# Kernel optimization log

Hardware: AMD Instinct MI355X
Metric: run time of the kernel (lower is better)

Reference implementation:

```python
import jax, jax.numpy as jnp
import numpy as np

EPS = 1e-8
LAM = 1.0


def setup_inputs() -> dict:
    key = jax.random.key(0)
    k1, k2 = jax.random.split(key)
    B, H, W = 32, 512, 512
    output = jax.random.normal(k1, (B, 1, H, W), dtype=jnp.float32)
    target = jax.random.normal(k2, (B, 1, H, W), dtype=jnp.float32)
    return {"output": output, "target": target}


def _frc_loss(output, target):
    # squeeze channel dim: (B,1,H,W) -> (B,H,W)
    output = output[:, 0]
    target = target[:, 0]
    B, H, W = output.shape
    rnyquist = H // 2

    # radial index map (H,W): round(sqrt(fx^2 + fy^2)) in pixel-frequency units
    fx = jnp.fft.fftfreq(H, 1.0 / H)
    fy = jnp.fft.fftfreq(W, 1.0 / W)
    X, Y = jnp.meshgrid(fx, fy, indexing='ij')
    radial = jnp.round(jnp.sqrt(X ** 2 + Y ** 2)).astype(jnp.int32)
    # bins > rnyquist were ignored by the original loop -> dump into extra bin
    idx = jnp.where(radial > rnyquist, rnyquist + 1, radial).reshape(-1)  # (H*W,)

    F1 = jnp.fft.fft2(output, norm='forward')  # (B,H,W) complex
    F2 = jnp.fft.fft2(target, norm='forward')

    # per-pixel correlation terms, laid out (HW, B) for segment_sum over leading axis
    a = (F1.real * F2.real + F1.imag * F2.imag).reshape(B, -1).T
    b = (F1.imag * F2.real - F1.real * F2.imag).reshape(B, -1).T
    c1 = (F1.real ** 2 + F1.imag ** 2).reshape(B, -1).T
    c2 = (F2.real ** 2 + F2.imag ** 2).reshape(B, -1).T
    stacked = jnp.stack([a, b, c1, c2], axis=-1)  # (HW, B, 4)

    # single-pass radial-bin segment sum (replaces O(R*H*W) masked loop)
    sums = jax.ops.segment_sum(stacked, idx, num_segments=rnyquist + 2)
    sums = sums[:rnyquist + 1]  # drop overflow bin -> (rnyquist+1, B, 4)
    C_r, C_i, C1, C2 = sums[..., 0], sums[..., 1], sums[..., 2], sums[..., 3]

    frc = jnp.sqrt(C_r ** 2 + C_i ** 2) / (jnp.sqrt(C1 * C2) + EPS)
    return LAM * jnp.mean((1.0 - frc) ** 2)


def reference(output, target):
    return _frc_loss(output, target)
```

## Files before the change

### kernel.cpp

```cpp
#include <hip/hip_runtime.h>
#include <math.h>

#define NIMG 32
#define NB3  771
#define PI_F 3.14159265358979323846f

__device__ __forceinline__ float2 cadd(float2 a, float2 b){ return make_float2(a.x+b.x, a.y+b.y); }
__device__ __forceinline__ float2 csub(float2 a, float2 b){ return make_float2(a.x-b.x, a.y-b.y); }
__device__ __forceinline__ float2 cmul(float2 a, float2 b){ return make_float2(a.x*b.x - a.y*b.y, a.x*b.y + a.y*b.x); }
__device__ __forceinline__ float2 cmul_mi(float2 a){ return make_float2(a.y, -a.x); }
__device__ __forceinline__ float2 tw(const float2* T, int m){ return T[m + (m >> 3)]; }
__device__ __forceinline__ int   sw(int pos){ return pos + (pos >> 3); }

__device__ __forceinline__ void dft8(float2* x) {
    const float c = 0.70710678118654752f;
    float2 u0 = cadd(x[0], x[4]), u1 = cadd(x[1], x[5]);
    float2 u2 = cadd(x[2], x[6]), u3 = cadd(x[3], x[7]);
    float2 v0 = csub(x[0], x[4]);
    float2 d1 = csub(x[1], x[5]);
    float2 v1 = make_float2(c*(d1.x + d1.y), c*(d1.y - d1.x));
    float2 d2 = csub(x[2], x[6]);
    float2 v2 = make_float2(d2.y, -d2.x);
    float2 d3 = csub(x[3], x[7]);
    float2 v3 = make_float2(-c*(d3.x - d3.y), -c*(d3.x + d3.y));
    float2 e0 = cadd(u0,u2), e1 = cadd(u1,u3);
    float2 f0 = csub(u0,u2), f1 = cmul_mi(csub(u1,u3));
    float2 g0 = cadd(v0,v2), g1 = cadd(v1,v3);
    float2 h0 = csub(v0,v2), h1 = cmul_mi(csub(v1,v3));
    x[0] = cadd(e0,e1); x[4] = csub(e0,e1);
    x[2] = cadd(f0,f1); x[6] = csub(f0,f1);
    x[1] = cadd(g0,g1); x[5] = csub(g0,g1);
    x[3] = cadd(h0,h1); x[7] = csub(h0,h1);
}

__device__ __forceinline__ void wave_fft512(float2* X, float2* Sw,
                                            const float2* T, int J) {
    dft8(X);
#pragma unroll
    for (int k = 1; k < 8; ++k) X[k] = cmul(X[k], tw(T, J * k));
    const int jj = J + (J >> 3);
#pragma unroll
    for (int k = 0; k < 8; ++k) Sw[jj + 72*k] = X[k];

    const int j2 = J & 7;
    const int bb = 72 * (J >> 3) + j2;
#pragma unroll
    for (int q = 0; q < 8; ++q) X[q] = Sw[bb + 9*q];
    dft8(X);
#pragma unroll
    for (int k = 1; k < 8; ++k) X[k] = cmul(X[k], tw(T, 8 * j2 * k));
#pragma unroll
    for (int k = 0; k < 8; ++k) Sw[bb + 9*k] = X[k];

#pragma unroll
    for (int q = 0; q < 8; ++q) X[q] = Sw[9*J + q];
    dft8(X);
}

__global__ __launch_bounds__(256, 6) void fft_rows_T(const float* __restrict__ xr,
                                                     const float* __restrict__ yr,
                                                     float2* __restrict__ Zt) {
    __shared__ float2 S[4 * 576];
    __shared__ float2 T[576];
    const int t = threadIdx.x, w = t >> 6, J = t & 63;
    const int im = blockIdx.x >> 6, grp = blockIdx.x & 63;

#pragma unroll
    for (int i = 0; i < 2; ++i) {
        const int m = t + 256 * i;
        float s, c;
        __sincosf(-2.0f * PI_F * (float)m / 512.0f, &s, &c);
        T[m + (m >> 3)] = make_float2(c, s);
    }

    const size_t b0 = ((size_t)(im * 512 + grp * 8 + w)) << 9;
    const size_t b1 = b0 + (4u << 9);
    float2 X0[8], X1[8];
#pragma unroll
    for (int q = 0; q < 8; ++q) {
        X0[q] = make_float2(xr[b0 + J + 64*q], yr[b0 + J + 64*q]);
        X1[q] = make_float2(xr[b1 + J + 64*q], yr[b1 + J + 64*q]);
    }
    __syncthreads();

    float2* Sw = S + w * 576;
    wave_fft512(X0, Sw, T, J);
    wave_fft512(X1, Sw, T, J);

    const int r = ((J & 7) << 3) | (J >> 3);

#pragma unroll
    for (int k = 0; k < 8; ++k) Sw[64*k + r] = X0[k];
    __syncthreads();
    float2 eA[4], eB[4];
#pragma unroll
    for (int j = 0; j < 4; ++j) { eA[j] = S[j*576 + t]; eB[j] = S[j*576 + t + 256]; }
    __syncthreads();

#pragma unroll
    for (int k = 0; k < 8; ++k) Sw[64*k + r] = X1[k];
    __syncthreads();

    const size_t zb = ((size_t)im << 18) + (grp << 3);
    {
        float4* o = (float4*)(Zt + zb + ((size_t)t << 9));
        float2 f0 = S[0*576 + t], f1 = S[1*576 + t];
        float2 f2 = S[2*576 + t], f3 = S[3*576 + t];
        o[0] = make_float4(eA[0].x, eA[0].y, eA[1].x, eA[1].y);
        o[1] = make_float4(eA[2].x, eA[2].y, eA[3].x, eA[3].y);
        o[2] = make_float4(f0.x, f0.y, f1.x, f1.y);
        o[3] = make_float4(f2.x, f2.y, f3.x, f3.y);
    }
    {
        float4* o = (float4*)(Zt + zb + ((size_t)(t + 256) << 9));
        float2 f0 = S[0*576 + t + 256], f1 = S[1*576 + t + 256];
        float2 f2 = S[2*576 + t + 256], f3 = S[3*576 + t + 256];
        o[0] = make_float4(eB[0].x, eB[0].y, eB[1].x, eB[1].y);
        o[1] = make_float4(eB[2].x, eB[2].y, eB[3].x, eB[3].y);
        o[2] = make_float4(f0.x, f0.y, f1.x, f1.y);
        o[3] = make_float4(f2.x, f2.y, f3.x, f3.y);
    }
}

__global__ __launch_bounds__(256) void fft_cols_rings(const float2* __restrict__ Zt,
                                                      float* __restrict__ sums,
                                                      int big) {
    __shared__ float2 S[8 * 576];
    __shared__ float2 T[576];
    __shared__ float  bins[258 * 3];
    const int t = threadIdx.x, w = t >> 6, J = t & 63;
    const int im = blockIdx.x >> 6, g = blockIdx.x & 63;
    const int p = 4 * g + w;

#pragma unroll
    for (int i = 0; i < 2; ++i) {
        const int m = t + 256 * i;
        float s, c;
        __sincosf(-2.0f * PI_F * (float)m / 512.0f, &s, &c);
        T[m + (m >> 3)] = make_float2(c, s);
    }
    for (int i = t; i < 258 * 3; i += 256) bins[i] = 0.0f;

    const int c0 = (p == 0) ? 0   : p;
    const int c1 = (p == 0) ? 256 : 512 - p;
    const float2* rp0 = Zt + ((size_t)im << 18) + ((size_t)c0 << 9);
    const float2* rp1 = Zt + ((size_t)im << 18) + ((size_t)c1 << 9);
    float2 X0[8], X1[8];
#pragma unroll
    for (int q = 0; q < 8; ++q) { X0[q] = rp0[J + 64*q]; X1[q] = rp1[J + 64*q]; }
    __syncthreads();

    float2* A = S + (2*w) * 576;
    float2* B = A + 576;
    const int r  = ((J & 7) << 3) | (J >> 3);
    const int pk = r + (r >> 3);

    wave_fft512(X0, A, T, J);
#pragma unroll
    for (int k = 0; k < 8; ++k) A[72*k + pk] = X0[k];
    wave_fft512(X1, B, T, J);
#pragma unroll
    for (int k = 0; k < 8; ++k) B[72*k + pk] = X1[k];

    const float scale = 1.0f / (512.0f * 512.0f);
    auto pix = [&](float2 zk, float2 zm, float& av, float& c1v, float& c2v) {
        float f1r = 0.5f * (zk.x + zm.x) * scale;
        float f1i = 0.5f * (zk.y - zm.y) * scale;
        float f2r = 0.5f * (zk.y + zm.y) * scale;
        float f2i = 0.5f * (zm.x - zk.x) * scale;
        av  = f1r * f2r + f1i * f2i;
        c1v = f1r * f1r + f1i * f1i;
        c2v = f2r * f2r + f2i * f2i;
    };
    auto flush = [&](int ring, float a, float b, float c) {
        if (ring >= 0 && ring <= 256) {
            unsafeAtomicAdd(&bins[ring*3+0], a);
            unsafeAtomicAdd(&bins[ring*3+1], b);
            unsafeAtomicAdd(&bins[ring*3+2], c);
        }
    };

    if (p == 0) {
        int cur0 = -1, cur1 = -1;
        float a0 = 0, b0 = 0, c0v = 0, a1 = 0, b1 = 0, c1v = 0;
#pragma unroll
        for (int i = 0; i < 8; ++i) {
            const int ky  = 8*J + i;
            const int kyp = (512 - ky) & 511;
            float2 zk0 = A[sw(ky)], zm0 = A[sw(kyp)];
            float2 zk1 = B[sw(ky)], zm1 = B[sw(kyp)];
            const float fk = (ky < 256) ? (float)ky : (float)(ky - 512);
            float av, cv, dv;
            pix(zk0, zm0, av, cv, dv);
            int rr = (int)rintf(fabsf(fk)); if (rr > 256) rr = 257;
            if (rr != cur0) { flush(cur0, a0, b0, c0v); cur0 = rr; a0 = av; b0 = cv; c0v = dv; }
            else            { a0 += av; b0 += cv; c0v += dv; }
            pix(zk1, zm1, av, cv, dv);
            rr = (int)rintf(sqrtf(fk*fk + 65536.0f)); if (rr > 256) rr = 257;
            if (rr != cur1) { flush(cur1, a1, b1, c1v); cur1 = rr; a1 = av; b1 = cv; c1v = dv; }
            else            { a1 += av; b1 += cv; c1v += dv; }
        }
        flush(cur0, a0, b0, c0v);
        flush(cur1, a1, b1, c1v);
    } else {
        const float fy2 = (float)p * (float)p;
        int curR = -1;
        float sA = 0, sB = 0, sC = 0;
#pragma unroll
        for (int i = 0; i < 8; ++i) {
            const int ky  = 8*J + i;
            const int kyp = (512 - ky) & 511;
            float2 zk = A[sw(ky)];
            float2 zm = B[sw(kyp)];
            float a1v, b1v, d1v, a2v, b2v, d2v;
            pix(zk, zm, a1v, b1v, d1v);
            pix(zm, zk, a2v, b2v, d2v);
            const float fk = (ky < 256) ? (float)ky : (float)(ky - 512);
            int rr = (int)rintf(sqrtf(fk*fk + fy2)); if (rr > 256) rr = 257;
            const float aa = a1v + a2v, bb = b1v + b2v, cc = d1v + d2v;
            if (rr != curR) { flush(curR, sA, sB, sC); curR = rr; sA = aa; sB = bb; sC = cc; }
            else            { sA += aa; sB += bb; sC += cc; }
        }
        flush(curR, sA, sB, sC);
    }
    __syncthreads();

    if (big) {
        float* dst = sums + (size_t)blockIdx.x * NB3;
        for (int i = t; i < NB3; i += 256) dst[i] = bins[i];
    } else {
        float* dst = sums + (size_t)(im * 8 + (g & 7)) * NB3;
        for (int i = t; i < NB3; i += 256) unsafeAtomicAdd(&dst[i], bins[i]);
    }
}

__global__ __launch_bounds__(256) void finalize(const float* __restrict__ sums,
                                                float* __restrict__ out, int spi) {
    const int b = blockIdx.x, t = threadIdx.x;
    float acc = 0.0f;
    for (int r = t; r < 257; r += 256) {
        float cr = 0.f, c1 = 0.f, c2 = 0.f;
        for (int s = 0; s < spi; ++s) {
            const float* pp = sums + (size_t)(b * spi + s) * NB3 + r * 3;
            cr += pp[0]; c1 += pp[1]; c2 += pp[2];
        }
        float frc = fabsf(cr) / (sqrtf(c1 * c2) + 1e-8f);
        float d = 1.0f - frc;
        acc += d * d;
    }
#pragma unroll
    for (int off = 32; off > 0; off >>= 1) acc += __shfl_down(acc, off);
    __shared__ float red[4];
    if ((t & 63) == 0) red[t >> 6] = acc;
    __syncthreads();
    if (t == 0)
        unsafeAtomicAdd(out, (red[0] + red[1] + red[2] + red[3]) *
                             (1.0f / (257.0f * (float)NIMG)));
}

extern "C" void kernel_launch(void* const* d_in, const int* in_sizes, int n_in,
                              void* d_out, int out_size, void* d_ws, size_t ws_size,
                              hipStream_t stream) {
    const float* xr = (const float*)d_in[0];
    const float* yr = (const float*)d_in[1];

    float2* Zt = (float2*)d_ws;
    const size_t ztBytes = ((size_t)NIMG << 18) * sizeof(float2);
    float* sums = (float*)((char*)d_ws + ztBytes);
    const int big = (ws_size >= ztBytes + (size_t)2048 * NB3 * sizeof(float)) ? 1 : 0;

    if (!big)
        hipMemsetAsync(sums, 0, (size_t)NIMG * 8 * NB3 * sizeof(float), stream);
    hipMemsetAsync(d_out, 0, sizeof(float), stream);

    fft_rows_T    <<<dim3(NIMG * 64), dim3(256), 0, stream>>>(xr, yr, Zt);
    fft_cols_rings<<<dim3(NIMG * 64), dim3(256), 0, stream>>>(Zt, sums, big);
    finalize      <<<dim3(NIMG), dim3(256), 0, stream>>>(sums, (float*)d_out, big ? 64 : 8);
}
```

Before: 213.9 us.

## Fuse row FFT, column FFT/ring binning and finalize into one persistent kernel

Replaces the three kernel launches and the memsets of sums and output with a single persistent kernel of 512 blocks. The blocks loop over the work units of each stage and meet at software grid barriers built from atomic counters in global memory. This removes launch gaps and the separate memset work, and always uses the atomic 8-slot sums path. The barriers only work if all 512 blocks are resident at once, which is not guaranteed, so the kernel can deadlock. Each stage also now runs at lower parallelism than the earlier 2048-block launches.

Measured after the change: 290.3 us. 1.36x slower.

```diff
diff --git a/kernel.cpp b/kernel.cpp
--- a/kernel.cpp
+++ b/kernel.cpp
@@ -4,13 +4,14 @@
 #define NIMG 32
 #define NB3  771
 #define PI_F 3.14159265358979323846f
+#define GRID 512
 
 __device__ __forceinline__ float2 cadd(float2 a, float2 b){ return make_float2(a.x+b.x, a.y+b.y); }
 __device__ __forceinline__ float2 csub(float2 a, float2 b){ return make_float2(a.x-b.x, a.y-b.y); }
 __device__ __forceinline__ float2 cmul(float2 a, float2 b){ return make_float2(a.x*b.x - a.y*b.y, a.x*b.y + a.y*b.x); }
 __device__ __forceinline__ float2 cmul_mi(float2 a){ return make_float2(a.y, -a.x); }
 __device__ __forceinline__ float2 tw(const float2* T, int m){ return T[m + (m >> 3)]; }
-__device__ __forceinline__ int   sw(int pos){ return pos + (pos >> 3); }
+__device__ __forceinline__ int   swz(int pos){ return pos + (pos >> 3); }
 
 __device__ __forceinline__ void dft8(float2* x) {
     const float c = 0.70710678118654752f;
@@ -57,13 +58,30 @@
     dft8(X);
 }
 
-__global__ __launch_bounds__(256, 6) void fft_rows_T(const float* __restrict__ xr,
-                                                     const float* __restrict__ yr,
-                                                     float2* __restrict__ Zt) {
-    __shared__ float2 S[4 * 576];
+__device__ __forceinline__ void gbar(unsigned* bar, int idx) {
+    __syncthreads();
+    if (threadIdx.x == 0) {
+        __threadfence();
+        atomicAdd(&bar[idx], 1u);
+        while (__hip_atomic_load(&bar[idx], __ATOMIC_RELAXED,
+                                 __HIP_MEMORY_SCOPE_AGENT) < GRID) {
+            __builtin_amdgcn_s_sleep(2);
+        }
+        __threadfence();
+    }
+    __syncthreads();
+}
+
+__global__ __launch_bounds__(256, 2)
+void frc_mega(const float* __restrict__ xr, const float* __restrict__ yr,
+              float2* __restrict__ Zt, float* __restrict__ sums,
+              unsigned* __restrict__ bar, float* __restrict__ out) {
+    __shared__ float2 S[8 * 576];
     __shared__ float2 T[576];
+    __shared__ float  bins[258 * 3];
+    __shared__ float  red[4];
     const int t = threadIdx.x, w = t >> 6, J = t & 63;
-    const int im = blockIdx.x >> 6, grp = blockIdx.x & 63;
+    const int r = ((J & 7) << 3) | (J >> 3);
 
 #pragma unroll
     for (int i = 0; i < 2; ++i) {
@@ -72,190 +90,175 @@
         __sincosf(-2.0f * PI_F * (float)m / 512.0f, &s, &c);
         T[m + (m >> 3)] = make_float2(c, s);
     }
-
-    const size_t b0 = ((size_t)(im * 512 + grp * 8 + w)) << 9;
-    const size_t b1 = b0 + (4u << 9);
-    float2 X0[8], X1[8];
-#pragma unroll
-    for (int q = 0; q < 8; ++q) {
-        X0[q] = make_float2(xr[b0 + J + 64*q], yr[b0 + J + 64*q]);
-        X1[q] = make_float2(xr[b1 + J + 64*q], yr[b1 + J + 64*q]);
-    }
+    for (int i = blockIdx.x * 256 + t; i < NIMG * 8 * NB3; i += GRID * 256)
+        sums[i] = 0.0f;
+    if (blockIdx.x == 0 && t == 0) atomicExch(out, 0.0f);
     __syncthreads();
 
-    float2* Sw = S + w * 576;
-    wave_fft512(X0, Sw, T, J);
-    wave_fft512(X1, Sw, T, J);
-
-    const int r = ((J & 7) << 3) | (J >> 3);
-
-#pragma unroll
-    for (int k = 0; k < 8; ++k) Sw[64*k + r] = X0[k];
-    __syncthreads();
-    float2 eA[4], eB[4];
-#pragma unroll
-    for (int j = 0; j < 4; ++j) { eA[j] = S[j*576 + t]; eB[j] = S[j*576 + t + 256]; }
-    __syncthreads();
-
-#pragma unroll
-    for (int k = 0; k < 8; ++k) Sw[64*k + r] = X1[k];
-    __syncthreads();
-
-    const size_t zb = ((size_t)im << 18) + (grp << 3);
-    {
-        float4* o = (float4*)(Zt + zb + ((size_t)t << 9));
-        float2 f0 = S[0*576 + t], f1 = S[1*576 + t];
-        float2 f2 = S[2*576 + t], f3 = S[3*576 + t];
-        o[0] = make_float4(eA[0].x, eA[0].y, eA[1].x, eA[1].y);
-        o[1] = make_float4(eA[2].x, eA[2].y, eA[3].x, eA[3].y);
-        o[2] = make_float4(f0.x, f0.y, f1.x, f1.y);
-        o[3] = make_float4(f2.x, f2.y, f3.x, f3.y);
-    }
-    {
-        float4* o = (float4*)(Zt + zb + ((size_t)(t + 256) << 9));
-        float2 f0 = S[0*576 + t + 256], f1 = S[1*576 + t + 256];
-        float2 f2 = S[2*576 + t + 256], f3 = S[3*576 + t + 256];
-        o[0] = make_float4(eB[0].x, eB[0].y, eB[1].x, eB[1].y);
-        o[1] = make_float4(eB[2].x, eB[2].y, eB[3].x, eB[3].y);
-        o[2] = make_float4(f0.x, f0.y, f1.x, f1.y);
-        o[3] = make_float4(f2.x, f2.y, f3.x, f3.y);
-    }
-}
-
-__global__ __launch_bounds__(256) void fft_cols_rings(const float2* __restrict__ Zt,
-                                                      float* __restrict__ sums,
-                                                      int big) {
-    __shared__ float2 S[8 * 576];
-    __shared__ float2 T[576];
-    __shared__ float  bins[258 * 3];
-    const int t = threadIdx.x, w = t >> 6, J = t & 63;
-    const int im = blockIdx.x >> 6, g = blockIdx.x & 63;
-    const int p = 4 * g + w;
-
-#pragma unroll
-    for (int i = 0; i < 2; ++i) {
-        const int m = t + 256 * i;
-        float s, c;
-        __sincosf(-2.0f * PI_F * (float)m / 512.0f, &s, &c);
-        T[m + (m >> 3)] = make_float2(c, s);
-    }
-    for (int i = t; i < 258 * 3; i += 256) bins[i] = 0.0f;
-
-    const int c0 = (p == 0) ? 0   : p;
-    const int c1 = (p == 0) ? 256 : 512 - p;
-    const float2* rp0 = Zt + ((size_t)im << 18) + ((size_t)c0 << 9);
-    const float2* rp1 = Zt + ((size_t)im << 18) + ((size_t)c1 << 9);
-    float2 X0[8], X1[8];
-#pragma unroll
-    for (int q = 0; q < 8; ++q) { X0[q] = rp0[J + 64*q]; X1[q] = rp1[J + 64*q]; }
-    __syncthreads();
-
-    float2* A = S + (2*w) * 576;
-    float2* B = A + 576;
-    const int r  = ((J & 7) << 3) | (J >> 3);
-    const int pk = r + (r >> 3);
-
-    wave_fft512(X0, A, T, J);
-#pragma unroll
-    for (int k = 0; k < 8; ++k) A[72*k + pk] = X0[k];
-    wave_fft512(X1, B, T, J);
-#pragma unroll
-    for (int k = 0; k < 8; ++k) B[72*k + pk] = X1[k];
+    for (int u = blockIdx.x; u < 2048; u += GRID) {
+        const int im = u >> 6, grp = u & 63;
+        const size_t b0 = ((size_t)(im * 512 + grp * 8 + w)) << 9;
+        const size_t b1 = b0 + 2048;
+        float2 X0[8], X1[8];
+#pragma unroll
+        for (int q = 0; q < 8; ++q) {
+            X0[q] = make_float2(xr[b0 + J + 64*q], yr[b0 + J + 64*q]);
+            X1[q] = make_float2(xr[b1 + J + 64*q], yr[b1 + J + 64*q]);
+        }
+        float2* Sw = S + w * 576;
+        wave_fft512(X0, Sw, T, J);
+        wave_fft512(X1, Sw, T, J);
+
+#pragma unroll
+        for (int k = 0; k < 8; ++k) Sw[64*k + r] = X0[k];
+        __syncthreads();
+        float2 eA[4], eB[4];
+#pragma unroll
+        for (int j = 0; j < 4; ++j) { eA[j] = S[j*576 + t]; eB[j] = S[j*576 + t + 256]; }
+        __syncthreads();
+#pragma unroll
+        for (int k = 0; k < 8; ++k) Sw[64*k + r] = X1[k];
+        __syncthreads();
+
+        const size_t zb = ((size_t)im << 18) + (grp << 3);
+        {
+            float4* o = (float4*)(Zt + zb + ((size_t)t << 9));
+            float2 f0 = S[0*576 + t], f1 = S[1*576 + t];
+            float2 f2 = S[2*576 + t], f3 = S[3*576 + t];
+            o[0] = make_float4(eA[0].x, eA[0].y, eA[1].x, eA[1].y);
+            o[1] = make_float4(eA[2].x, eA[2].y, eA[3].x, eA[3].y);
+            o[2] = make_float4(f0.x, f0.y, f1.x, f1.y);
+            o[3] = make_float4(f2.x, f2.y, f3.x, f3.y);
+        }
+        {
+            float4* o = (float4*)(Zt + zb + ((size_t)(t + 256) << 9));
+            float2 f0 = S[0*576 + t + 256], f1 = S[1*576 + t + 256];
+            float2 f2 = S[2*576 + t + 256], f3 = S[3*576 + t + 256];
+            o[0] = make_float4(eB[0].x, eB[0].y, eB[1].x, eB[1].y);
+            o[1] = make_float4(eB[2].x, eB[2].y, eB[3].x, eB[3].y);
+            o[2] = make_float4(f0.x, f0.y, f1.x, f1.y);
+            o[3] = make_float4(f2.x, f2.y, f3.x, f3.y);
+        }
+        __syncthreads();
+    }
+
+    gbar(bar, 0);
 
     const float scale = 1.0f / (512.0f * 512.0f);
-    auto pix = [&](float2 zk, float2 zm, float& av, float& c1v, float& c2v) {
-        float f1r = 0.5f * (zk.x + zm.x) * scale;
-        float f1i = 0.5f * (zk.y - zm.y) * scale;
-        float f2r = 0.5f * (zk.y + zm.y) * scale;
-        float f2i = 0.5f * (zm.x - zk.x) * scale;
-        av  = f1r * f2r + f1i * f2i;
-        c1v = f1r * f1r + f1i * f1i;
-        c2v = f2r * f2r + f2i * f2i;
-    };
-    auto flush = [&](int ring, float a, float b, float c) {
-        if (ring >= 0 && ring <= 256) {
-            unsafeAtomicAdd(&bins[ring*3+0], a);
-            unsafeAtomicAdd(&bins[ring*3+1], b);
-            unsafeAtomicAdd(&bins[ring*3+2], c);
-        }
-    };
-
-    if (p == 0) {
-        int cur0 = -1, cur1 = -1;
-        float a0 = 0, b0 = 0, c0v = 0, a1 = 0, b1 = 0, c1v = 0;
-#pragma unroll
-        for (int i = 0; i < 8; ++i) {
-            const int ky  = 8*J + i;
-            const int kyp = (512 - ky) & 511;
-            float2 zk0 = A[sw(ky)], zm0 = A[sw(kyp)];
-            float2 zk1 = B[sw(ky)], zm1 = B[sw(kyp)];
-            const float fk = (ky < 256) ? (float)ky : (float)(ky - 512);
-            float av, cv, dv;
-            pix(zk0, zm0, av, cv, dv);
-            int rr = (int)rintf(fabsf(fk)); if (rr > 256) rr = 257;
-            if (rr != cur0) { flush(cur0, a0, b0, c0v); cur0 = rr; a0 = av; b0 = cv; c0v = dv; }
-            else            { a0 += av; b0 += cv; c0v += dv; }
-            pix(zk1, zm1, av, cv, dv);
-            rr = (int)rintf(sqrtf(fk*fk + 65536.0f)); if (rr > 256) rr = 257;
-            if (rr != cur1) { flush(cur1, a1, b1, c1v); cur1 = rr; a1 = av; b1 = cv; c1v = dv; }
-            else            { a1 += av; b1 += cv; c1v += dv; }
-        }
-        flush(cur0, a0, b0, c0v);
-        flush(cur1, a1, b1, c1v);
-    } else {
-        const float fy2 = (float)p * (float)p;
-        int curR = -1;
-        float sA = 0, sB = 0, sC = 0;
-#pragma unroll
-        for (int i = 0; i < 8; ++i) {
-            const int ky  = 8*J + i;
-            const int kyp = (512 - ky) & 511;
-            float2 zk = A[sw(ky)];
-            float2 zm = B[sw(kyp)];
-            float a1v, b1v, d1v, a2v, b2v, d2v;
-            pix(zk, zm, a1v, b1v, d1v);
-            pix(zm, zk, a2v, b2v, d2v);
-            const float fk = (ky < 256) ? (float)ky : (float)(ky - 512);
-            int rr = (int)rintf(sqrtf(fk*fk + fy2)); if (rr > 256) rr = 257;
-            const float aa = a1v + a2v, bb = b1v + b2v, cc = d1v + d2v;
-            if (rr != curR) { flush(curR, sA, sB, sC); curR = rr; sA = aa; sB = bb; sC = cc; }
-            else            { sA += aa; sB += bb; sC += cc; }
-        }
-        flush(curR, sA, sB, sC);
-    }
-    __syncthreads();
-
-    if (big) {
-        float* dst = sums + (size_t)blockIdx.x * NB3;
-        for (int i = t; i < NB3; i += 256) dst[i] = bins[i];
-    } else {
+    for (int u = blockIdx.x; u < 2048; u += GRID) {
+        const int im = u >> 6, g = u & 63;
+        const int p = 4 * g + w;
+        for (int i = t; i < 258 * 3; i += 256) bins[i] = 0.0f;
+
+        const int c0 = (p == 0) ? 0   : p;
+        const int c1 = (p == 0) ? 256 : 512 - p;
+        const float2* rp0 = Zt + ((size_t)im << 18) + ((size_t)c0 << 9);
+        const float2* rp1 = Zt + ((size_t)im << 18) + ((size_t)c1 << 9);
+        float2 X0[8], X1[8];
+#pragma unroll
+        for (int q = 0; q < 8; ++q) { X0[q] = rp0[J + 64*q]; X1[q] = rp1[J + 64*q]; }
+        __syncthreads();
+
+        float2* A = S + (2*w) * 576;
+        float2* B = A + 576;
+        const int pk = r + (r >> 3);
+        wave_fft512(X0, A, T, J);
+#pragma unroll
+        for (int k = 0; k < 8; ++k) A[72*k + pk] = X0[k];
+        wave_fft512(X1, B, T, J);
+#pragma unroll
+        for (int k = 0; k < 8; ++k) B[72*k + pk] = X1[k];
+
+        auto pix = [&](float2 zk, float2 zm, float& av, float& c1v, float& c2v) {
+            float f1r = 0.5f * (zk.x + zm.x) * scale;
+            float f1i = 0.5f * (zk.y - zm.y) * scale;
+            float f2r = 0.5f * (zk.y + zm.y) * scale;
+            float f2i = 0.5f * (zm.x - zk.x) * scale;
+            av  = f1r * f2r + f1i * f2i;
+            c1v = f1r * f1r + f1i * f1i;
+            c2v = f2r * f2r + f2i * f2i;
+        };
+        auto flush = [&](int ring, float a, float b, float c) {
+            if (ring >= 0 && ring <= 256) {
+                unsafeAtomicAdd(&bins[ring*3+0], a);
+                unsafeAtomicAdd(&bins[ring*3+1], b);
+                unsafeAtomicAdd(&bins[ring*3+2], c);
+            }
+        };
+
+        if (p == 0) {
+            int cur0 = -1, cur1 = -1;
+            float a0 = 0, b0 = 0, c0v = 0, a1 = 0, b1 = 0, c1v = 0;
+#pragma unroll
+            for (int i = 0; i < 8; ++i) {
+                const int ky  = 8*J + i;
+                const int kyp = (512 - ky) & 511;
+                float2 zk0 = A[swz(ky)], zm0 = A[swz(kyp)];
+                float2 zk1 = B[swz(ky)], zm1 = B[swz(kyp)];
+                const float fk = (ky < 256) ? (float)ky : (float)(ky - 512);
+                float av, cv, dv;
+                pix(zk0, zm0, av, cv, dv);
+                int rr = (int)rintf(fabsf(fk)); if (rr > 256) rr = 257;
+                if (rr != cur0) { flush(cur0, a0, b0, c0v); cur0 = rr; a0 = av; b0 = cv; c0v = dv; }
+                else            { a0 += av; b0 += cv; c0v += dv; }
+                pix(zk1, zm1, av, cv, dv);
+                rr = (int)rintf(sqrtf(fk*fk + 65536.0f)); if (rr > 256) rr = 257;
+                if (rr != cur1) { flush(cur1, a1, b1, c1v); cur1 = rr; a1 = av; b1 = cv; c1v = dv; }
+                else            { a1 += av; b1 += cv; c1v += dv; }
+            }
+            flush(cur0, a0, b0, c0v);
+            flush(cur1, a1, b1, c1v);
+        } else {
+            const float fy2 = (float)p * (float)p;
+            int curR = -1;
+            float sA = 0, sB = 0, sC = 0;
+#pragma unroll
+            for (int i = 0; i < 8; ++i) {
+                const int ky  = 8*J + i;
+                const int kyp = (512 - ky) & 511;
+                float2 zk = A[swz(ky)];
+                float2 zm = B[swz(kyp)];
+                float a1v, b1v, d1v, a2v, b2v, d2v;
+                pix(zk, zm, a1v, b1v, d1v);
+                pix(zm, zk, a2v, b2v, d2v);
+                const float fk = (ky < 256) ? (float)ky : (float)(ky - 512);
+                int rr = (int)rintf(sqrtf(fk*fk + fy2)); if (rr > 256) rr = 257;
+                const float aa = a1v + a2v, bb = b1v + b2v, cc = d1v + d2v;
+                if (rr != curR) { flush(curR, sA, sB, sC); curR = rr; sA = aa; sB = bb; sC = cc; }
+                else            { sA += aa; sB += bb; sC += cc; }
+            }
+            flush(curR, sA, sB, sC);
+        }
+        __syncthreads();
         float* dst = sums + (size_t)(im * 8 + (g & 7)) * NB3;
         for (int i = t; i < NB3; i += 256) unsafeAtomicAdd(&dst[i], bins[i]);
-    }
-}
-
-__global__ __launch_bounds__(256) void finalize(const float* __restrict__ sums,
-                                                float* __restrict__ out, int spi) {
-    const int b = blockIdx.x, t = threadIdx.x;
-    float acc = 0.0f;
-    for (int r = t; r < 257; r += 256) {
-        float cr = 0.f, c1 = 0.f, c2 = 0.f;
-        for (int s = 0; s < spi; ++s) {
-            const float* pp = sums + (size_t)(b * spi + s) * NB3 + r * 3;
-            cr += pp[0]; c1 += pp[1]; c2 += pp[2];
-        }
-        float frc = fabsf(cr) / (sqrtf(c1 * c2) + 1e-8f);
-        float d = 1.0f - frc;
-        acc += d * d;
-    }
-#pragma unroll
-    for (int off = 32; off > 0; off >>= 1) acc += __shfl_down(acc, off);
-    __shared__ float red[4];
-    if ((t & 63) == 0) red[t >> 6] = acc;
-    __syncthreads();
-    if (t == 0)
-        unsafeAtomicAdd(out, (red[0] + red[1] + red[2] + red[3]) *
-                             (1.0f / (257.0f * (float)NIMG)));
+        __syncthreads();
+    }
+
+    gbar(bar, 1);
+
+    if (blockIdx.x < NIMG) {
+        const int im = blockIdx.x;
+        float acc = 0.0f;
+        for (int rr = t; rr < 257; rr += 256) {
+            float cr = 0.f, c1 = 0.f, c2 = 0.f;
+#pragma unroll
+            for (int s = 0; s < 8; ++s) {
+                const float* pp = sums + (size_t)(im * 8 + s) * NB3 + rr * 3;
+                cr += pp[0]; c1 += pp[1]; c2 += pp[2];
+            }
+            float frc = fabsf(cr) / (sqrtf(c1 * c2) + 1e-8f);
+            float d = 1.0f - frc;
+            acc += d * d;
+        }
+#pragma unroll
+        for (int off = 32; off > 0; off >>= 1) acc += __shfl_down(acc, off);
+        if ((t & 63) == 0) red[t >> 6] = acc;
+        __syncthreads();
+        if (t == 0)
+            unsafeAtomicAdd(out, (red[0] + red[1] + red[2] + red[3]) *
+                                 (1.0f / (257.0f * (float)NIMG)));
+    }
 }
 
 extern "C" void kernel_launch(void* const* d_in, const int* in_sizes, int n_in,
@@ -264,16 +267,12 @@
     const float* xr = (const float*)d_in[0];
     const float* yr = (const float*)d_in[1];
 
-    float2* Zt = (float2*)d_ws;
-    const size_t ztBytes = ((size_t)NIMG << 18) * sizeof(float2);
-    float* sums = (float*)((char*)d_ws + ztBytes);
-    const int big = (ws_size >= ztBytes + (size_t)2048 * NB3 * sizeof(float)) ? 1 : 0;
-
-    if (!big)
-        hipMemsetAsync(sums, 0, (size_t)NIMG * 8 * NB3 * sizeof(float), stream);
-    hipMemsetAsync(d_out, 0, sizeof(float), stream);
-
-    fft_rows_T    <<<dim3(NIMG * 64), dim3(256), 0, stream>>>(xr, yr, Zt);
-    fft_cols_rings<<<dim3(NIMG * 64), dim3(256), 0, stream>>>(Zt, sums, big);
-    finalize      <<<dim3(NIMG), dim3(256), 0, stream>>>(sums, (float*)d_out, big ? 64 : 8);
-}
+    float2*   Zt   = (float2*)d_ws;
+    float*    sums = (float*)((char*)d_ws + (((size_t)NIMG << 18) * sizeof(float2)));
+    unsigned* bar  = (unsigned*)(sums + (size_t)NIMG * 8 * NB3);
+    float*    out  = (float*)d_out;
+
+    hipMemsetAsync(bar, 0, 2 * sizeof(unsigned), stream);
+
+    frc_mega<<<dim3(GRID), dim3(256), 0, stream>>>(xr, yr, Zt, sums, bar, out);
+}
```

## Vectorize global loads via LDS staging, fold memsets into kernels, single-block finalize

Applied to the files above, without the earlier changes.

Global reads in both FFT kernels now use float4 loads and are redistributed to the per-wave FFT layout through the padded shared-memory buffer, replacing the strided scalar/float2 loads. The memset of the partial-sum buffer moves into the row-FFT kernel, and the output memset and atomic are removed by having a single finalize block write the result directly. Launch bounds change to an occupancy hint of 4 for both FFT kernels. The extra LDS round trips add shared-memory traffic, and the single-block finalize serializes the last reduction.

Measured after the change: 735.9 us. +244.0%, slower.

```diff
diff --git a/kernel.cpp b/kernel.cpp
--- a/kernel.cpp
+++ b/kernel.cpp
@@ -10,7 +10,7 @@
 __device__ __forceinline__ float2 cmul(float2 a, float2 b){ return make_float2(a.x*b.x - a.y*b.y, a.x*b.y + a.y*b.x); }
 __device__ __forceinline__ float2 cmul_mi(float2 a){ return make_float2(a.y, -a.x); }
 __device__ __forceinline__ float2 tw(const float2* T, int m){ return T[m + (m >> 3)]; }
-__device__ __forceinline__ int   sw(int pos){ return pos + (pos >> 3); }
+__device__ __forceinline__ int   swz(int pos){ return pos + (pos >> 3); }
 
 __device__ __forceinline__ void dft8(float2* x) {
     const float c = 0.70710678118654752f;
@@ -57,9 +57,11 @@
     dft8(X);
 }
 
-__global__ __launch_bounds__(256, 6) void fft_rows_T(const float* __restrict__ xr,
+__global__ __launch_bounds__(256, 4) void fft_rows_T(const float* __restrict__ xr,
                                                      const float* __restrict__ yr,
-                                                     float2* __restrict__ Zt) {
+                                                     float2* __restrict__ Zt,
+                                                     float* __restrict__ sums,
+                                                     int big) {
     __shared__ float2 S[4 * 576];
     __shared__ float2 T[576];
     const int t = threadIdx.x, w = t >> 6, J = t & 63;
@@ -72,18 +74,46 @@
         __sincosf(-2.0f * PI_F * (float)m / 512.0f, &s, &c);
         T[m + (m >> 3)] = make_float2(c, s);
     }
+    if (!big) {
+        const int idx = blockIdx.x * 256 + t;
+        if (idx < NIMG * 8 * NB3) sums[idx] = 0.0f;
+    }
 
     const size_t b0 = ((size_t)(im * 512 + grp * 8 + w)) << 9;
-    const size_t b1 = b0 + (4u << 9);
+    const float4* x40 = (const float4*)(xr + b0);
+    const float4* y40 = (const float4*)(yr + b0);
+    const float4* x41 = (const float4*)(xr + b0 + 2048);
+    const float4* y41 = (const float4*)(yr + b0 + 2048);
+    float4 aX0 = x40[J], aX1 = x40[J + 64];
+    float4 aY0 = y40[J], aY1 = y40[J + 64];
+    float4 bX0 = x41[J], bX1 = x41[J + 64];
+    float4 bY0 = y41[J], bY1 = y41[J + 64];
+    __syncthreads();
+
+    float2* Sw = S + w * 576;
     float2 X0[8], X1[8];
-#pragma unroll
-    for (int q = 0; q < 8; ++q) {
-        X0[q] = make_float2(xr[b0 + J + 64*q], yr[b0 + J + 64*q]);
-        X1[q] = make_float2(xr[b1 + J + 64*q], yr[b1 + J + 64*q]);
-    }
-    __syncthreads();
-
-    float2* Sw = S + w * 576;
+
+    {
+        const int p0 = 4 * J,        s0 = p0 + (p0 >> 3);
+        const int p1 = 4 * J + 256,  s1 = p1 + (p1 >> 3);
+        Sw[s0+0] = make_float2(aX0.x, aY0.x); Sw[s0+1] = make_float2(aX0.y, aY0.y);
+        Sw[s0+2] = make_float2(aX0.z, aY0.z); Sw[s0+3] = make_float2(aX0.w, aY0.w);
+        Sw[s1+0] = make_float2(aX1.x, aY1.x); Sw[s1+1] = make_float2(aX1.y, aY1.y);
+        Sw[s1+2] = make_float2(aX1.z, aY1.z); Sw[s1+3] = make_float2(aX1.w, aY1.w);
+#pragma unroll
+        for (int q = 0; q < 8; ++q) X0[q] = Sw[swz(J + 64*q)];
+    }
+    {
+        const int p0 = 4 * J,        s0 = p0 + (p0 >> 3);
+        const int p1 = 4 * J + 256,  s1 = p1 + (p1 >> 3);
+        Sw[s0+0] = make_float2(bX0.x, bY0.x); Sw[s0+1] = make_float2(bX0.y, bY0.y);
+        Sw[s0+2] = make_float2(bX0.z, bY0.z); Sw[s0+3] = make_float2(bX0.w, bY0.w);
+        Sw[s1+0] = make_float2(bX1.x, bY1.x); Sw[s1+1] = make_float2(bX1.y, bY1.y);
+        Sw[s1+2] = make_float2(bX1.z, bY1.z); Sw[s1+3] = make_float2(bX1.w, bY1.w);
+#pragma unroll
+        for (int q = 0; q < 8; ++q) X1[q] = Sw[swz(J + 64*q)];
+    }
+
     wave_fft512(X0, Sw, T, J);
     wave_fft512(X1, Sw, T, J);
 
@@ -96,7 +126,6 @@
 #pragma unroll
     for (int j = 0; j < 4; ++j) { eA[j] = S[j*576 + t]; eB[j] = S[j*576 + t + 256]; }
     __syncthreads();
-
 #pragma unroll
     for (int k = 0; k < 8; ++k) Sw[64*k + r] = X1[k];
     __syncthreads();
@@ -122,9 +151,9 @@
     }
 }
 
-__global__ __launch_bounds__(256) void fft_cols_rings(const float2* __restrict__ Zt,
-                                                      float* __restrict__ sums,
-                                                      int big) {
+__global__ __launch_bounds__(256, 4) void fft_cols_rings(const float2* __restrict__ Zt,
+                                                         float* __restrict__ sums,
+                                                         int big) {
     __shared__ float2 S[8 * 576];
     __shared__ float2 T[576];
     __shared__ float  bins[258 * 3];
@@ -143,21 +172,38 @@
 
     const int c0 = (p == 0) ? 0   : p;
     const int c1 = (p == 0) ? 256 : 512 - p;
-    const float2* rp0 = Zt + ((size_t)im << 18) + ((size_t)c0 << 9);
-    const float2* rp1 = Zt + ((size_t)im << 18) + ((size_t)c1 << 9);
-    float2 X0[8], X1[8];
-#pragma unroll
-    for (int q = 0; q < 8; ++q) { X0[q] = rp0[J + 64*q]; X1[q] = rp1[J + 64*q]; }
+    const float4* f40 = (const float4*)(Zt + ((size_t)im << 18) + ((size_t)c0 << 9));
+    const float4* f41 = (const float4*)(Zt + ((size_t)im << 18) + ((size_t)c1 << 9));
+    float4 L0[4], L1[4];
+#pragma unroll
+    for (int i = 0; i < 4; ++i) { L0[i] = f40[J + 64*i]; L1[i] = f41[J + 64*i]; }
     __syncthreads();
 
     float2* A = S + (2*w) * 576;
     float2* B = A + 576;
     const int r  = ((J & 7) << 3) | (J >> 3);
     const int pk = r + (r >> 3);
-
+    float2 X0[8], X1[8];
+
+#pragma unroll
+    for (int i = 0; i < 4; ++i) {
+        const int pp = 2 * (J + 64*i), ss = pp + (pp >> 3);
+        A[ss]   = make_float2(L0[i].x, L0[i].y);
+        A[ss+1] = make_float2(L0[i].z, L0[i].w);
+    }
+#pragma unroll
+    for (int q = 0; q < 8; ++q) X0[q] = A[swz(J + 64*q)];
     wave_fft512(X0, A, T, J);
 #pragma unroll
     for (int k = 0; k < 8; ++k) A[72*k + pk] = X0[k];
+#pragma unroll
+    for (int i = 0; i < 4; ++i) {
+        const int pp = 2 * (J + 64*i), ss = pp + (pp >> 3);
+        B[ss]   = make_float2(L1[i].x, L1[i].y);
+        B[ss+1] = make_float2(L1[i].z, L1[i].w);
+    }
+#pragma unroll
+    for (int q = 0; q < 8; ++q) X1[q] = B[swz(J + 64*q)];
     wave_fft512(X1, B, T, J);
 #pragma unroll
     for (int k = 0; k < 8; ++k) B[72*k + pk] = X1[k];
@@ -187,8 +233,8 @@
         for (int i = 0; i < 8; ++i) {
             const int ky  = 8*J + i;
             const int kyp = (512 - ky) & 511;
-            float2 zk0 = A[sw(ky)], zm0 = A[sw(kyp)];
-            float2 zk1 = B[sw(ky)], zm1 = B[sw(kyp)];
+            float2 zk0 = A[swz(ky)], zm0 = A[swz(kyp)];
+            float2 zk1 = B[swz(ky)], zm1 = B[swz(kyp)];
             const float fk = (ky < 256) ? (float)ky : (float)(ky - 512);
             float av, cv, dv;
             pix(zk0, zm0, av, cv, dv);
@@ -210,8 +256,8 @@
         for (int i = 0; i < 8; ++i) {
             const int ky  = 8*J + i;
             const int kyp = (512 - ky) & 511;
-            float2 zk = A[sw(ky)];
-            float2 zm = B[sw(kyp)];
+            float2 zk = A[swz(ky)];
+            float2 zm = B[swz(kyp)];
             float a1v, b1v, d1v, a2v, b2v, d2v;
             pix(zk, zm, a1v, b1v, d1v);
             pix(zm, zk, a2v, b2v, d2v);
@@ -235,13 +281,15 @@
 }
 
 __global__ __launch_bounds__(256) void finalize(const float* __restrict__ sums,
-                                                float* __restrict__ out, int spi) {
-    const int b = blockIdx.x, t = threadIdx.x;
+                                                float* __restrict__ out, int nsl) {
+    const int t = threadIdx.x;
     float acc = 0.0f;
-    for (int r = t; r < 257; r += 256) {
+    for (int i = t; i < 257 * NIMG; i += 256) {
+        const int rr = i % 257;
+        const int im = i / 257;
         float cr = 0.f, c1 = 0.f, c2 = 0.f;
-        for (int s = 0; s < spi; ++s) {
-            const float* pp = sums + (size_t)(b * spi + s) * NB3 + r * 3;
+        for (int s = 0; s < nsl; ++s) {
+            const float* pp = sums + (size_t)(im * nsl + s) * NB3 + rr * 3;
             cr += pp[0]; c1 += pp[1]; c2 += pp[2];
         }
         float frc = fabsf(cr) / (sqrtf(c1 * c2) + 1e-8f);
@@ -254,8 +302,7 @@
     if ((t & 63) == 0) red[t >> 6] = acc;
     __syncthreads();
     if (t == 0)
-        unsafeAtomicAdd(out, (red[0] + red[1] + red[2] + red[3]) *
-                             (1.0f / (257.0f * (float)NIMG)));
+        out[0] = (red[0] + red[1] + red[2] + red[3]) * (1.0f / (257.0f * (float)NIMG));
 }
 
 extern "C" void kernel_launch(void* const* d_in, const int* in_sizes, int n_in,
@@ -269,11 +316,7 @@
     float* sums = (float*)((char*)d_ws + ztBytes);
     const int big = (ws_size >= ztBytes + (size_t)2048 * NB3 * sizeof(float)) ? 1 : 0;
 
-    if (!big)
-        hipMemsetAsync(sums, 0, (size_t)NIMG * 8 * NB3 * sizeof(float), stream);
-    hipMemsetAsync(d_out, 0, sizeof(float), stream);
-
-    fft_rows_T    <<<dim3(NIMG * 64), dim3(256), 0, stream>>>(xr, yr, Zt);
+    fft_rows_T    <<<dim3(NIMG * 64), dim3(256), 0, stream>>>(xr, yr, Zt, sums, big);
     fft_cols_rings<<<dim3(NIMG * 64), dim3(256), 0, stream>>>(Zt, sums, big);
-    finalize      <<<dim3(NIMG), dim3(256), 0, stream>>>(sums, (float*)d_out, big ? 64 : 8);
-}
+    finalize      <<<dim3(1), dim3(256), 0, stream>>>(sums, (float*)d_out, big ? 64 : 8);
+}
```
